# Performance work log

Measured on AMD Instinct MI355X. Metric: run time of the kernel, lower is better.

## Reference

```python
import jax, jax.numpy as jnp
import numpy as np

D_K = 8192   # sequence length (module calls it d_k)
D_MODEL = 128

def setup_inputs() -> dict:
    key = jax.random.key(0)
    k1, k2, k3 = jax.random.split(key, 3)
    Q = jax.random.normal(k1, (D_K, D_MODEL), dtype=jnp.float32)
    K = jax.random.normal(k2, (D_K, D_MODEL), dtype=jnp.float32)
    V = jax.random.normal(k3, (D_K, D_MODEL), dtype=jnp.float32)
    return {"Q": Q, "K": K, "V": V}

def reference(Q, K, V):
    # scores: [d_k, d_k] -- full attention matrix, scaled by 1/sqrt(d_k)
    # (faithful to the source: scale uses d_k, the sequence dim)
    inv_scale = 1.0 / jnp.sqrt(jnp.asarray(D_K, dtype=Q.dtype))
    scores = jnp.einsum('qd,kd->qk', Q, K) * inv_scale
    attn = jax.nn.softmax(scores, axis=-1)
    return jnp.einsum('qk,kd->qd', attn, V)
```

## Files before the change

kernel.cpp:

```cpp
#include <hip/hip_runtime.h>

#define SEQ 8192
#define DM  128
#define KS  8

typedef __attribute__((ext_vector_type(8)))  short bf16x8;
typedef __attribute__((ext_vector_type(16))) float f32x16;

static __device__ __forceinline__ unsigned short f2bf(float f) {
    unsigned int u = __builtin_bit_cast(unsigned int, f);
    u += 0x7FFFu + ((u >> 16) & 1u);
    return (unsigned short)(u >> 16);
}
static __device__ __forceinline__ unsigned int pack2bf(float a, float b) {
    return ((unsigned int)f2bf(b) << 16) | (unsigned int)f2bf(a);
}
static __device__ __forceinline__ float bflo(unsigned int u) {
    return __builtin_bit_cast(float, u << 16);
}
static __device__ __forceinline__ float bfhi(unsigned int u) {
    return __builtin_bit_cast(float, u & 0xFFFF0000u);
}
static __device__ __forceinline__ bf16x8 as_frag(uint4 v) {
    return __builtin_bit_cast(bf16x8, v);
}
static __device__ __forceinline__ unsigned int pack2bf_trunc(float a, float b) {
    return __builtin_amdgcn_perm(__builtin_bit_cast(unsigned int, b),
                                 __builtin_bit_cast(unsigned int, a), 0x07060302u);
}
static __device__ __forceinline__ void gl_lds16(const void* g, void* l) {
    __builtin_amdgcn_global_load_lds(
        (const __attribute__((address_space(1))) void*)(unsigned long long)g,
        (__attribute__((address_space(3))) void*)(unsigned int)(unsigned long long)l,
        16, 0, 0);
}
#define CL2 (1.4426950408889634f / 90.50966799187809f)

__global__ __launch_bounds__(256) void prep_kernel(
        const float* __restrict__ Q, const float* __restrict__ K,
        const float* __restrict__ V,
        uint2* __restrict__ Qb2, uint4* __restrict__ Kt, uint4* __restrict__ Vt) {
    __shared__ float VL[32 * 132 + 4];
    const int b = blockIdx.x, tid = threadIdx.x;
    const float4* Q4 = (const float4*)Q;
    const float4* K4 = (const float4*)K;
    const float4* V4 = (const float4*)V;

    #pragma unroll
    for (int u = 0; u < 4; ++u) {
        int f4 = u * 256 + tid;
        int k = f4 >> 5, c4 = f4 & 31;
        float4 v = V4[(size_t)b * 1024 + f4];
        *(float4*)(VL + k * 132 + c4 * 4) = v;
    }
    #pragma unroll
    for (int u = 0; u < 4; ++u) {
        int f4 = u * 256 + tid;
        float4 v = Q4[(size_t)b * 1024 + f4];
        Qb2[(size_t)b * 1024 + f4] = make_uint2(pack2bf(v.x * CL2, v.y * CL2),
                                                pack2bf(v.z * CL2, v.w * CL2));
    }
    #pragma unroll
    for (int u = 0; u < 2; ++u) {
        int p = u * 256 + tid;
        int q = p & 31, h = (p >> 5) & 1, s = p >> 6;
        int fi = ((size_t)0, (b * 32 + q) * 32 + s * 4 + h * 2);
        float4 a = K4[fi], c = K4[fi + 1];
        Kt[(size_t)b * 512 + p] = make_uint4(pack2bf(a.x, a.y), pack2bf(a.z, a.w),
                                             pack2bf(c.x, c.y), pack2bf(c.z, c.w));
    }
    __syncthreads();
    #pragma unroll
    for (int u = 0; u < 2; ++u) {
        int p = u * 256 + tid;
        int q = p & 31, h = (p >> 5) & 1, w = p >> 6;
        int d = (w >> 1) * 32 + q;
        int k0 = (w & 1) * 16 + h * 8;
        unsigned int r[4];
        #pragma unroll
        for (int jj = 0; jj < 4; ++jj) {
            float e0 = VL[(k0 + 2 * jj) * 132 + d];
            float e1 = VL[(k0 + 2 * jj + 1) * 132 + d];
            r[jj] = pack2bf(e0, e1);
        }
        Vt[(size_t)b * 512 + p] = make_uint4(r[0], r[1], r[2], r[3]);
    }
}

__global__ __launch_bounds__(512, 2) void attn_kernel(
        const unsigned short* __restrict__ Qb,
        const uint4* __restrict__ Kt,
        const uint4* __restrict__ Vt,
        uint2* __restrict__ Opart, float* __restrict__ Lpart) {
    __shared__ __align__(16) char smem[65536];
    __shared__ float Lx[128];
    const int tid = threadIdx.x;
    const int wid = tid >> 6, lane = tid & 63;
    const int i = wid & 3, j = wid >> 2;
    const int q = lane & 31, h = lane >> 5;
    const int qt = blockIdx.x & 63, ks = blockIdx.x >> 6;
    const int qbase = qt * 128 + i * 32;
    const int tile0 = ks * 32 + j * 16;

    uint4 qf[8];
    {
        const unsigned short* qrow = Qb + (qbase + q) * DM + 8 * h;
        #pragma unroll
        for (int s = 0; s < 8; ++s) qf[s] = *(const uint4*)(qrow + 16 * s);
    }

    f32x16 oacc[4];
    #pragma unroll
    for (int mb = 0; mb < 4; ++mb)
        #pragma unroll
        for (int r = 0; r < 16; ++r) oacc[mb][r] = 0.f;
    float lsum = 0.f;

    char* const mybuf = smem + j * 32768;
    auto stage = [&](int buf, int tile) {
        char* base = mybuf + buf * 16384;
        const uint4* kt = Kt + (size_t)tile * 512;
        const uint4* vt = Vt + (size_t)tile * 512;
        #pragma unroll
        for (int u = 0; u < 2; ++u) {
            int ki = i * 2 + u;
            gl_lds16(kt + ki * 64 + lane, base + ki * 1024);
            gl_lds16(vt + ki * 64 + lane, base + 8192 + ki * 1024);
        }
    };

    stage(0, tile0);
    #pragma unroll 1
    for (int t = 0; t < 16; ++t) {
        __syncthreads();
        if (t < 15) stage((t + 1) & 1, tile0 + t + 1);
        const char* kl = mybuf + (t & 1) * 16384 + lane * 16;

        uint4 kf[8];
        #pragma unroll
        for (int s = 0; s < 8; ++s) kf[s] = *(const uint4*)(kl + s * 1024);

        f32x16 sacc;
        #pragma unroll
        for (int r = 0; r < 16; ++r) sacc[r] = 0.f;
        #pragma unroll
        for (int s = 0; s < 8; ++s)
            sacc = __builtin_amdgcn_mfma_f32_32x32x16_bf16(
                       as_frag(kf[s]), as_frag(qf[s]), sacc, 0, 0, 0);

        uint4 vf[8];
        #pragma unroll
        for (int w = 0; w < 8; ++w) vf[w] = *(const uint4*)(kl + 8192 + w * 1024);

        float p[16];
        #pragma unroll
        for (int r = 0; r < 16; ++r) {
            p[r] = __builtin_amdgcn_exp2f(sacc[r]);
            lsum += p[r];
        }
        unsigned int pk[8], px[8];
        #pragma unroll
        for (int jj = 0; jj < 8; ++jj) pk[jj] = pack2bf_trunc(p[2 * jj], p[2 * jj + 1]);
        #pragma unroll
        for (int jj = 0; jj < 8; ++jj) px[jj] = (unsigned int)__shfl_xor((int)pk[jj], 32);
        uint4 B0, B1;
        B0.x = h ? px[2] : pk[0];  B0.y = h ? px[3] : pk[1];
        B0.z = h ? pk[2] : px[0];  B0.w = h ? pk[3] : px[1];
        B1.x = h ? px[6] : pk[4];  B1.y = h ? px[7] : pk[5];
        B1.z = h ? pk[6] : px[4];  B1.w = h ? pk[7] : px[5];

        #pragma unroll
        for (int mb = 0; mb < 4; ++mb) {
            oacc[mb] = __builtin_amdgcn_mfma_f32_32x32x16_bf16(
                           as_frag(vf[mb * 2 + 0]), as_frag(B0), oacc[mb], 0, 0, 0);
            oacc[mb] = __builtin_amdgcn_mfma_f32_32x32x16_bf16(
                           as_frag(vf[mb * 2 + 1]), as_frag(B1), oacc[mb], 0, 0, 0);
        }
    }

    float l2 = lsum + __shfl_xor(lsum, 32);
    __syncthreads();
    float* Lg = (float*)(smem + i * 16384);
    if (j == 0) {
        #pragma unroll
        for (int mb = 0; mb < 4; ++mb)
            #pragma unroll
            for (int r = 0; r < 16; ++r) {
                int dl = 32 * mb + (r & 3) + 8 * (r >> 2) + 4 * h;
                Lg[dl * 32 + q] = oacc[mb][r];
            }
        if (h == 0) Lx[i * 32 + q] = l2;
    }
    __syncthreads();
    if (j == 1) {
        #pragma unroll
        for (int mb = 0; mb < 4; ++mb)
            #pragma unroll
            for (int r = 0; r < 16; ++r) {
                int dl = 32 * mb + (r & 3) + 8 * (r >> 2) + 4 * h;
                Lg[dl * 32 + q] += oacc[mb][r];
            }
        if (h == 0) Lpart[(size_t)ks * SEQ + qbase + q] = Lx[i * 32 + q] + l2;
    }
    __syncthreads();
    #pragma unroll
    for (int u = 0; u < 8; ++u) {
        int idx = u * 512 + tid;
        int rd = idx >> 5, c4 = idx & 31;
        int ig = c4 >> 3, q4 = c4 & 7;
        float4 v = *(const float4*)(smem + ig * 16384 + (rd * 8 + q4) * 16);
        Opart[(((size_t)(ks * 64 + qt)) * 128 + rd) * 32 + c4] =
            make_uint2(pack2bf(v.x, v.y), pack2bf(v.z, v.w));
    }
}

__global__ __launch_bounds__(256) void reduce_kernel(
        const uint2* __restrict__ Opart, const float* __restrict__ Lpart,
        float* __restrict__ Out) {
    __shared__ float T[32 * 132 + 4];
    __shared__ float Rinv[128];
    const int tid = threadIdx.x;
    const int qt = blockIdx.x & 63, dq = blockIdx.x >> 6;
    if (tid < 128) {
        float L = 0.f;
        #pragma unroll
        for (int ks = 0; ks < KS; ++ks) L += Lpart[(size_t)ks * SEQ + qt * 128 + tid];
        Rinv[tid] = 1.0f / L;
    }
    const int c = tid & 31, dsub = tid >> 5;
    float4 acc[4];
    #pragma unroll
    for (int rr = 0; rr < 4; ++rr) { acc[rr].x = acc[rr].y = acc[rr].z = acc[rr].w = 0.f; }
    #pragma unroll 1
    for (int ks = 0; ks < KS; ++ks) {
        #pragma unroll
        for (int rr = 0; rr < 4; ++rr) {
            int d_l = rr * 8 + dsub;
            uint2 w = Opart[(((size_t)(ks * 64 + qt)) * 128 + dq * 32 + d_l) * 32 + c];
            acc[rr].x += bflo(w.x); acc[rr].y += bfhi(w.x);
            acc[rr].z += bflo(w.y); acc[rr].w += bfhi(w.y);
        }
    }
    #pragma unroll
    for (int rr = 0; rr < 4; ++rr)
        *(float4*)(T + (rr * 8 + dsub) * 132 + c * 4) = acc[rr];
    __syncthreads();
    const int q_l = tid >> 1, hf = tid & 1;
    float r = Rinv[q_l];
    #pragma unroll
    for (int g = 0; g < 4; ++g) {
        float4 o;
        o.x = T[(hf * 16 + g * 4 + 0) * 132 + q_l] * r;
        o.y = T[(hf * 16 + g * 4 + 1) * 132 + q_l] * r;
        o.z = T[(hf * 16 + g * 4 + 2) * 132 + q_l] * r;
        o.w = T[(hf * 16 + g * 4 + 3) * 132 + q_l] * r;
        *(float4*)(Out + ((size_t)(qt * 128 + q_l)) * DM + dq * 32 + hf * 16 + g * 4) = o;
    }
}

extern "C" void kernel_launch(void* const* d_in, const int* in_sizes, int n_in,
                              void* d_out, int out_size, void* d_ws, size_t ws_size,
                              hipStream_t stream) {
    const float* Q = (const float*)d_in[0];
    const float* K = (const float*)d_in[1];
    const float* V = (const float*)d_in[2];
    char* ws = (char*)d_ws;
    uint2* Qb2  = (uint2*)ws;
    uint4* Kt   = (uint4*)(ws + 2 * 1024 * 1024);
    uint4* Vt   = (uint4*)(ws + 4 * 1024 * 1024);
    float* Lpart= (float*)(ws + 6 * 1024 * 1024);
    uint2* Opart= (uint2*)(ws + 6 * 1024 * 1024 + 262144);
    float* Out  = (float*)d_out;

    prep_kernel<<<256, 256, 0, stream>>>(Q, K, V, Qb2, Kt, Vt);
    attn_kernel<<<512, 512, 0, stream>>>((const unsigned short*)Qb2, Kt, Vt,
                                         Opart, Lpart);
    reduce_kernel<<<256, 256, 0, stream>>>(Opart, Lpart, Out);
}
```

Measured before the change: 117.0 us.

## Restructure attention: 64-query waves, interleaved K/V tiles, fragment-order partials

```diff
diff --git a/kernel.cpp b/kernel.cpp
--- a/kernel.cpp
+++ b/kernel.cpp
@@ -2,7 +2,7 @@
 
 #define SEQ 8192
 #define DM  128
-#define KS  8
+#define NKS 8
 
 typedef __attribute__((ext_vector_type(8)))  short bf16x8;
 typedef __attribute__((ext_vector_type(16))) float f32x16;
@@ -39,222 +39,227 @@
 __global__ __launch_bounds__(256) void prep_kernel(
         const float* __restrict__ Q, const float* __restrict__ K,
         const float* __restrict__ V,
-        uint2* __restrict__ Qb2, uint4* __restrict__ Kt, uint4* __restrict__ Vt) {
-    __shared__ float VL[32 * 132 + 4];
+        uint4* __restrict__ Qt, uint4* __restrict__ KV) {
+    __shared__ float TL[32 * 136];
     const int b = blockIdx.x, tid = threadIdx.x;
-    const float4* Q4 = (const float4*)Q;
-    const float4* K4 = (const float4*)K;
-    const float4* V4 = (const float4*)V;
-
+    const int which = b >> 8, tile = b & 255;
+    const float4* S4 = (which == 0) ? (const float4*)Q
+                     : (which == 1) ? (const float4*)K : (const float4*)V;
     #pragma unroll
     for (int u = 0; u < 4; ++u) {
         int f4 = u * 256 + tid;
         int k = f4 >> 5, c4 = f4 & 31;
-        float4 v = V4[(size_t)b * 1024 + f4];
-        *(float4*)(VL + k * 132 + c4 * 4) = v;
-    }
-    #pragma unroll
-    for (int u = 0; u < 4; ++u) {
-        int f4 = u * 256 + tid;
-        float4 v = Q4[(size_t)b * 1024 + f4];
-        Qb2[(size_t)b * 1024 + f4] = make_uint2(pack2bf(v.x * CL2, v.y * CL2),
-                                                pack2bf(v.z * CL2, v.w * CL2));
-    }
-    #pragma unroll
-    for (int u = 0; u < 2; ++u) {
-        int p = u * 256 + tid;
-        int q = p & 31, h = (p >> 5) & 1, s = p >> 6;
-        int fi = ((size_t)0, (b * 32 + q) * 32 + s * 4 + h * 2);
-        float4 a = K4[fi], c = K4[fi + 1];
-        Kt[(size_t)b * 512 + p] = make_uint4(pack2bf(a.x, a.y), pack2bf(a.z, a.w),
-                                             pack2bf(c.x, c.y), pack2bf(c.z, c.w));
-    }
-    __syncthreads();
-    #pragma unroll
-    for (int u = 0; u < 2; ++u) {
-        int p = u * 256 + tid;
-        int q = p & 31, h = (p >> 5) & 1, w = p >> 6;
-        int d = (w >> 1) * 32 + q;
-        int k0 = (w & 1) * 16 + h * 8;
-        unsigned int r[4];
-        #pragma unroll
-        for (int jj = 0; jj < 4; ++jj) {
-            float e0 = VL[(k0 + 2 * jj) * 132 + d];
-            float e1 = VL[(k0 + 2 * jj + 1) * 132 + d];
-            r[jj] = pack2bf(e0, e1);
-        }
-        Vt[(size_t)b * 512 + p] = make_uint4(r[0], r[1], r[2], r[3]);
-    }
-}
-
-__global__ __launch_bounds__(512, 2) void attn_kernel(
-        const unsigned short* __restrict__ Qb,
-        const uint4* __restrict__ Kt,
-        const uint4* __restrict__ Vt,
-        uint2* __restrict__ Opart, float* __restrict__ Lpart) {
-    __shared__ __align__(16) char smem[65536];
-    __shared__ float Lx[128];
+        float4 v = S4[(size_t)tile * 1024 + f4];
+        *(float4*)(TL + k * 136 + c4 * 4) = v;
+    }
+    __syncthreads();
+    if (which < 2) {
+        const float scale = (which == 0) ? (float)CL2 : 1.0f;
+        uint4* dst = (which == 0) ? (Qt + (size_t)tile * 512)
+                                  : (KV + (size_t)tile * 1024);
+        #pragma unroll
+        for (int u = 0; u < 2; ++u) {
+            int p = u * 256 + tid;
+            int q = p & 31, h = (p >> 5) & 1, s = p >> 6;
+            const float* src = TL + q * 136 + s * 16 + h * 8;
+            float4 a = *(const float4*)(src);
+            float4 c = *(const float4*)(src + 4);
+            dst[p] = make_uint4(pack2bf(a.x * scale, a.y * scale),
+                                pack2bf(a.z * scale, a.w * scale),
+                                pack2bf(c.x * scale, c.y * scale),
+                                pack2bf(c.z * scale, c.w * scale));
+        }
+    } else {
+        uint4* dst = KV + (size_t)tile * 1024 + 512;
+        #pragma unroll
+        for (int u = 0; u < 2; ++u) {
+            int p = u * 256 + tid;
+            int q = p & 31, h = (p >> 5) & 1, p64 = p >> 6;
+            int d = (p64 >> 1) * 32 + q;
+            int k0 = (p64 & 1) * 16 + h * 8;
+            unsigned int r[4];
+            #pragma unroll
+            for (int jj = 0; jj < 4; ++jj)
+                r[jj] = pack2bf(TL[(k0 + 2 * jj) * 136 + d],
+                                TL[(k0 + 2 * jj + 1) * 136 + d]);
+            dst[p] = make_uint4(r[0], r[1], r[2], r[3]);
+        }
+    }
+}
+
+__global__ __launch_bounds__(256, 2) void attn_kernel(
+        const uint4* __restrict__ Qt, const uint4* __restrict__ KV,
+        unsigned short* __restrict__ Opart, float* __restrict__ Lpart) {
+    __shared__ __align__(16) uint4 kvbuf[2][2][1024];
+    __shared__ float Lw[4][64];
     const int tid = threadIdx.x;
-    const int wid = tid >> 6, lane = tid & 63;
-    const int i = wid & 3, j = wid >> 2;
+    const int w = tid >> 6, lane = tid & 63;
     const int q = lane & 31, h = lane >> 5;
-    const int qt = blockIdx.x & 63, ks = blockIdx.x >> 6;
-    const int qbase = qt * 128 + i * 32;
-    const int tile0 = ks * 32 + j * 16;
-
-    uint4 qf[8];
+    const int wq = w & 1, ss = w >> 1;
+    const int ks = blockIdx.x & 7, qt = blockIdx.x >> 3;
+    const int sub = qt * 2 + wq;
+
+    uint4 qf0[8], qf1[8];
     {
-        const unsigned short* qrow = Qb + (qbase + q) * DM + 8 * h;
-        #pragma unroll
-        for (int s = 0; s < 8; ++s) qf[s] = *(const uint4*)(qrow + 16 * s);
-    }
-
-    f32x16 oacc[4];
-    #pragma unroll
-    for (int mb = 0; mb < 4; ++mb)
-        #pragma unroll
-        for (int r = 0; r < 16; ++r) oacc[mb][r] = 0.f;
-    float lsum = 0.f;
-
-    char* const mybuf = smem + j * 32768;
-    auto stage = [&](int buf, int tile) {
-        char* base = mybuf + buf * 16384;
-        const uint4* kt = Kt + (size_t)tile * 512;
-        const uint4* vt = Vt + (size_t)tile * 512;
-        #pragma unroll
-        for (int u = 0; u < 2; ++u) {
-            int ki = i * 2 + u;
-            gl_lds16(kt + ki * 64 + lane, base + ki * 1024);
-            gl_lds16(vt + ki * 64 + lane, base + 8192 + ki * 1024);
-        }
+        const uint4* qs = Qt + (size_t)(2 * sub) * 512 + lane;
+        #pragma unroll
+        for (int s = 0; s < 8; ++s) { qf0[s] = qs[s * 64]; qf1[s] = qs[512 + s * 64]; }
+    }
+
+    f32x16 oacc[8];
+    #pragma unroll
+    for (int a = 0; a < 8; ++a)
+        #pragma unroll
+        for (int r = 0; r < 16; ++r) oacc[a][r] = 0.f;
+    float ls0 = 0.f, ls1 = 0.f;
+
+    const uint4* kv0 = KV + ((size_t)(ks * 32 + ss * 16)) * 1024 + wq * 512;
+    auto stage = [&](int buf, int t) {
+        const uint4* src = kv0 + (size_t)t * 1024;
+        uint4* dst = &kvbuf[ss][buf][wq * 512];
+        #pragma unroll
+        for (int u = 0; u < 8; ++u)
+            gl_lds16(src + u * 64 + lane, dst + u * 64);
     };
 
-    stage(0, tile0);
+    stage(0, 0);
+    __syncthreads();
     #pragma unroll 1
     for (int t = 0; t < 16; ++t) {
+        if (t < 15) stage((t + 1) & 1, t + 1);
+        const uint4* kb = &kvbuf[ss][t & 1][0];
+
+        f32x16 s0, s1;
+        #pragma unroll
+        for (int r = 0; r < 16; ++r) { s0[r] = 0.f; s1[r] = 0.f; }
+        #pragma unroll
+        for (int s = 0; s < 8; ++s) {
+            uint4 kf = kb[s * 64 + lane];
+            s0 = __builtin_amdgcn_mfma_f32_32x32x16_bf16(as_frag(kf), as_frag(qf0[s]), s0, 0, 0, 0);
+            s1 = __builtin_amdgcn_mfma_f32_32x32x16_bf16(as_frag(kf), as_frag(qf1[s]), s1, 0, 0, 0);
+        }
+
+        #pragma unroll
+        for (int g = 0; g < 2; ++g) {
+            float p[16];
+            #pragma unroll
+            for (int r = 0; r < 16; ++r) {
+                float sv = g ? s1[r] : s0[r];
+                p[r] = __builtin_amdgcn_exp2f(sv);
+                if (g) ls1 += p[r]; else ls0 += p[r];
+            }
+            unsigned int pk[8], px[8];
+            #pragma unroll
+            for (int jj = 0; jj < 8; ++jj) pk[jj] = pack2bf_trunc(p[2 * jj], p[2 * jj + 1]);
+            #pragma unroll
+            for (int jj = 0; jj < 8; ++jj) px[jj] = (unsigned int)__shfl_xor((int)pk[jj], 32);
+            uint4 B0, B1;
+            B0.x = h ? px[2] : pk[0];  B0.y = h ? px[3] : pk[1];
+            B0.z = h ? pk[2] : px[0];  B0.w = h ? pk[3] : px[1];
+            B1.x = h ? px[6] : pk[4];  B1.y = h ? px[7] : pk[5];
+            B1.z = h ? pk[6] : px[4];  B1.w = h ? pk[7] : px[5];
+            #pragma unroll
+            for (int mb = 0; mb < 4; ++mb) {
+                uint4 va = kb[512 + (2 * mb) * 64 + lane];
+                uint4 vb = kb[512 + (2 * mb + 1) * 64 + lane];
+                oacc[g * 4 + mb] = __builtin_amdgcn_mfma_f32_32x32x16_bf16(
+                    as_frag(va), as_frag(B0), oacc[g * 4 + mb], 0, 0, 0);
+                oacc[g * 4 + mb] = __builtin_amdgcn_mfma_f32_32x32x16_bf16(
+                    as_frag(vb), as_frag(B1), oacc[g * 4 + mb], 0, 0, 0);
+            }
+        }
         __syncthreads();
-        if (t < 15) stage((t + 1) & 1, tile0 + t + 1);
-        const char* kl = mybuf + (t & 1) * 16384 + lane * 16;
-
-        uint4 kf[8];
-        #pragma unroll
-        for (int s = 0; s < 8; ++s) kf[s] = *(const uint4*)(kl + s * 1024);
-
-        f32x16 sacc;
-        #pragma unroll
-        for (int r = 0; r < 16; ++r) sacc[r] = 0.f;
-        #pragma unroll
-        for (int s = 0; s < 8; ++s)
-            sacc = __builtin_amdgcn_mfma_f32_32x32x16_bf16(
-                       as_frag(kf[s]), as_frag(qf[s]), sacc, 0, 0, 0);
-
-        uint4 vf[8];
-        #pragma unroll
-        for (int w = 0; w < 8; ++w) vf[w] = *(const uint4*)(kl + 8192 + w * 1024);
-
-        float p[16];
+    }
+
+    float l0 = ls0 + __shfl_xor(ls0, 32);
+    float l1 = ls1 + __shfl_xor(ls1, 32);
+    if (h == 0) { Lw[w][q] = l0; Lw[w][32 + q] = l1; }
+    if (w >= 2) {
+        float* D = (float*)&kvbuf[0][0][0] + (w - 2) * 8192;
+        #pragma unroll
+        for (int a = 0; a < 8; ++a)
+            #pragma unroll
+            for (int r = 0; r < 16; ++r)
+                D[(a * 16 + r) * 64 + lane] = oacc[a][r];
+    }
+    __syncthreads();
+    if (w < 2) {
+        const float* D = (const float*)&kvbuf[0][0][0] + w * 8192;
+        #pragma unroll
+        for (int a = 0; a < 8; ++a)
+            #pragma unroll
+            for (int r = 0; r < 16; ++r)
+                oacc[a][r] += D[(a * 16 + r) * 64 + lane];
+        if (h == 0) {
+            Lpart[ks * SEQ + sub * 64 + q]      = l0 + Lw[w + 2][q];
+            Lpart[ks * SEQ + sub * 64 + 32 + q] = l1 + Lw[w + 2][32 + q];
+        }
+        unsigned short* dst = Opart + ((size_t)(ks * 128 + sub)) * 8192 + lane * 16;
+        #pragma unroll
+        for (int a = 0; a < 8; ++a) {
+            unsigned int o[8];
+            #pragma unroll
+            for (int u = 0; u < 8; ++u)
+                o[u] = pack2bf(oacc[a][2 * u], oacc[a][2 * u + 1]);
+            *(uint4*)(dst + a * 1024)     = make_uint4(o[0], o[1], o[2], o[3]);
+            *(uint4*)(dst + a * 1024 + 8) = make_uint4(o[4], o[5], o[6], o[7]);
+        }
+    }
+}
+
+__global__ __launch_bounds__(256) void reduce_kernel(
+        const unsigned short* __restrict__ Opart, const float* __restrict__ Lpart,
+        float* __restrict__ Out) {
+    __shared__ float T[64 * 132];
+    __shared__ float Linv[64];
+    const int tid = threadIdx.x, sub = blockIdx.x;
+    if (tid < 64) {
+        float L = 0.f;
+        #pragma unroll
+        for (int ks = 0; ks < NKS; ++ks) L += Lpart[ks * SEQ + sub * 64 + tid];
+        Linv[tid] = 1.0f / L;
+    }
+    const int l = tid & 63, A = tid >> 6;
+    float acc[32];
+    #pragma unroll
+    for (int u = 0; u < 32; ++u) acc[u] = 0.f;
+    #pragma unroll 1
+    for (int ks = 0; ks < NKS; ++ks) {
+        const unsigned short* src = Opart + ((size_t)(ks * 128 + sub)) * 8192 + l * 16;
+        #pragma unroll
+        for (int ai = 0; ai < 2; ++ai) {
+            const uint4* s4 = (const uint4*)(src + (2 * A + ai) * 1024);
+            uint4 v0 = s4[0], v1 = *(const uint4*)((const unsigned short*)s4 + 8);
+            float* a = acc + ai * 16;
+            a[0] += bflo(v0.x);  a[1] += bfhi(v0.x);
+            a[2] += bflo(v0.y);  a[3] += bfhi(v0.y);
+            a[4] += bflo(v0.z);  a[5] += bfhi(v0.z);
+            a[6] += bflo(v0.w);  a[7] += bfhi(v0.w);
+            a[8] += bflo(v1.x);  a[9] += bfhi(v1.x);
+            a[10] += bflo(v1.y); a[11] += bfhi(v1.y);
+            a[12] += bflo(v1.z); a[13] += bfhi(v1.z);
+            a[14] += bflo(v1.w); a[15] += bfhi(v1.w);
+        }
+    }
+    const int hh = l >> 5;
+    #pragma unroll
+    for (int ai = 0; ai < 2; ++ai) {
+        int a = 2 * A + ai;
+        int q_loc = (a >> 2) * 32 + (l & 31);
         #pragma unroll
         for (int r = 0; r < 16; ++r) {
-            p[r] = __builtin_amdgcn_exp2f(sacc[r]);
-            lsum += p[r];
-        }
-        unsigned int pk[8], px[8];
-        #pragma unroll
-        for (int jj = 0; jj < 8; ++jj) pk[jj] = pack2bf_trunc(p[2 * jj], p[2 * jj + 1]);
-        #pragma unroll
-        for (int jj = 0; jj < 8; ++jj) px[jj] = (unsigned int)__shfl_xor((int)pk[jj], 32);
-        uint4 B0, B1;
-        B0.x = h ? px[2] : pk[0];  B0.y = h ? px[3] : pk[1];
-        B0.z = h ? pk[2] : px[0];  B0.w = h ? pk[3] : px[1];
-        B1.x = h ? px[6] : pk[4];  B1.y = h ? px[7] : pk[5];
-        B1.z = h ? pk[6] : px[4];  B1.w = h ? pk[7] : px[5];
-
-        #pragma unroll
-        for (int mb = 0; mb < 4; ++mb) {
-            oacc[mb] = __builtin_amdgcn_mfma_f32_32x32x16_bf16(
-                           as_frag(vf[mb * 2 + 0]), as_frag(B0), oacc[mb], 0, 0, 0);
-            oacc[mb] = __builtin_amdgcn_mfma_f32_32x32x16_bf16(
-                           as_frag(vf[mb * 2 + 1]), as_frag(B1), oacc[mb], 0, 0, 0);
-        }
-    }
-
-    float l2 = lsum + __shfl_xor(lsum, 32);
-    __syncthreads();
-    float* Lg = (float*)(smem + i * 16384);
-    if (j == 0) {
-        #pragma unroll
-        for (int mb = 0; mb < 4; ++mb)
-            #pragma unroll
-            for (int r = 0; r < 16; ++r) {
-                int dl = 32 * mb + (r & 3) + 8 * (r >> 2) + 4 * h;
-                Lg[dl * 32 + q] = oacc[mb][r];
-            }
-        if (h == 0) Lx[i * 32 + q] = l2;
-    }
-    __syncthreads();
-    if (j == 1) {
-        #pragma unroll
-        for (int mb = 0; mb < 4; ++mb)
-            #pragma unroll
-            for (int r = 0; r < 16; ++r) {
-                int dl = 32 * mb + (r & 3) + 8 * (r >> 2) + 4 * h;
-                Lg[dl * 32 + q] += oacc[mb][r];
-            }
-        if (h == 0) Lpart[(size_t)ks * SEQ + qbase + q] = Lx[i * 32 + q] + l2;
-    }
-    __syncthreads();
-    #pragma unroll
-    for (int u = 0; u < 8; ++u) {
-        int idx = u * 512 + tid;
-        int rd = idx >> 5, c4 = idx & 31;
-        int ig = c4 >> 3, q4 = c4 & 7;
-        float4 v = *(const float4*)(smem + ig * 16384 + (rd * 8 + q4) * 16);
-        Opart[(((size_t)(ks * 64 + qt)) * 128 + rd) * 32 + c4] =
-            make_uint2(pack2bf(v.x, v.y), pack2bf(v.z, v.w));
-    }
-}
-
-__global__ __launch_bounds__(256) void reduce_kernel(
-        const uint2* __restrict__ Opart, const float* __restrict__ Lpart,
-        float* __restrict__ Out) {
-    __shared__ float T[32 * 132 + 4];
-    __shared__ float Rinv[128];
-    const int tid = threadIdx.x;
-    const int qt = blockIdx.x & 63, dq = blockIdx.x >> 6;
-    if (tid < 128) {
-        float L = 0.f;
-        #pragma unroll
-        for (int ks = 0; ks < KS; ++ks) L += Lpart[(size_t)ks * SEQ + qt * 128 + tid];
-        Rinv[tid] = 1.0f / L;
-    }
-    const int c = tid & 31, dsub = tid >> 5;
-    float4 acc[4];
-    #pragma unroll
-    for (int rr = 0; rr < 4; ++rr) { acc[rr].x = acc[rr].y = acc[rr].z = acc[rr].w = 0.f; }
-    #pragma unroll 1
-    for (int ks = 0; ks < KS; ++ks) {
-        #pragma unroll
-        for (int rr = 0; rr < 4; ++rr) {
-            int d_l = rr * 8 + dsub;
-            uint2 w = Opart[(((size_t)(ks * 64 + qt)) * 128 + dq * 32 + d_l) * 32 + c];
-            acc[rr].x += bflo(w.x); acc[rr].y += bfhi(w.x);
-            acc[rr].z += bflo(w.y); acc[rr].w += bfhi(w.y);
-        }
-    }
-    #pragma unroll
-    for (int rr = 0; rr < 4; ++rr)
-        *(float4*)(T + (rr * 8 + dsub) * 132 + c * 4) = acc[rr];
-    __syncthreads();
-    const int q_l = tid >> 1, hf = tid & 1;
-    float r = Rinv[q_l];
-    #pragma unroll
-    for (int g = 0; g < 4; ++g) {
-        float4 o;
-        o.x = T[(hf * 16 + g * 4 + 0) * 132 + q_l] * r;
-        o.y = T[(hf * 16 + g * 4 + 1) * 132 + q_l] * r;
-        o.z = T[(hf * 16 + g * 4 + 2) * 132 + q_l] * r;
-        o.w = T[(hf * 16 + g * 4 + 3) * 132 + q_l] * r;
-        *(float4*)(Out + ((size_t)(qt * 128 + q_l)) * DM + dq * 32 + hf * 16 + g * 4) = o;
+            int d = (a & 3) * 32 + (r & 3) + 8 * (r >> 2) + 4 * hh;
+            T[q_loc * 132 + d] = acc[ai * 16 + r];
+        }
+    }
+    __syncthreads();
+    const int q_loc = tid >> 2, dseg = (tid & 3) * 32;
+    const float rv = Linv[q_loc];
+    #pragma unroll
+    for (int c = 0; c < 8; ++c) {
+        const float* tp = T + q_loc * 132 + dseg + c * 4;
+        float4 o = make_float4(tp[0] * rv, tp[1] * rv, tp[2] * rv, tp[3] * rv);
+        *(float4*)(Out + (size_t)(sub * 64 + q_loc) * DM + dseg + c * 4) = o;
     }
 }
 
@@ -265,15 +270,13 @@
     const float* K = (const float*)d_in[1];
     const float* V = (const float*)d_in[2];
     char* ws = (char*)d_ws;
-    uint2* Qb2  = (uint2*)ws;
-    uint4* Kt   = (uint4*)(ws + 2 * 1024 * 1024);
-    uint4* Vt   = (uint4*)(ws + 4 * 1024 * 1024);
-    float* Lpart= (float*)(ws + 6 * 1024 * 1024);
-    uint2* Opart= (uint2*)(ws + 6 * 1024 * 1024 + 262144);
-    float* Out  = (float*)d_out;
-
-    prep_kernel<<<256, 256, 0, stream>>>(Q, K, V, Qb2, Kt, Vt);
-    attn_kernel<<<512, 512, 0, stream>>>((const unsigned short*)Qb2, Kt, Vt,
-                                         Opart, Lpart);
-    reduce_kernel<<<256, 256, 0, stream>>>(Opart, Lpart, Out);
-}
+    uint4* Qt            = (uint4*)ws;
+    uint4* KV            = (uint4*)(ws + 2 * 1024 * 1024);
+    float* Lpart         = (float*)(ws + 6 * 1024 * 1024);
+    unsigned short* Opart= (unsigned short*)(ws + 6 * 1024 * 1024 + 262144);
+    float* Out = (float*)d_out;
+
+    prep_kernel<<<768, 256, 0, stream>>>(Q, K, V, Qt, KV);
+    attn_kernel<<<512, 256, 0, stream>>>(Qt, KV, Opart, Lpart);
+    reduce_kernel<<<128, 256, 0, stream>>>(Opart, Lpart, Out);
+}
```

Result: slower. 125.1 us (+6.9%).
